# Kernel tuning notes

Measured on AMD Instinct MI355X. Metric: run time of the kernel, lower is better.

The kernel has to match this reference:

```python
import jax, jax.numpy as jnp
import numpy as np

C0, C1, ED, H, L, K = 128, 32, 64, 4, 2, 16
RADIUS = 16.0
EPS = 1e-6


def _ln(x, g, b):
    m = jnp.mean(x, -1, keepdims=True)
    v = jnp.var(x, -1, keepdims=True)
    return (x - m) * jax.lax.rsqrt(v + 1e-5) * g + b


def _gather_nodes(x, idx):
    # x [B,N,...], idx [B,N,K] -> [B,N,K,...]
    return jax.vmap(lambda xb, ib: xb[ib])(x, idx)


def _gather_pairs(e, idx):
    # e [B,N,N,ED], idx [B,N,K] -> [B,N,K,ED]  (batched_index_select on dim=2)
    return jax.vmap(lambda eb, ib: jnp.take_along_axis(eb, ib[..., None], axis=1))(e, idx)


def _fiber_norm(f0, f1, g0, b0, g1, b1):
    # deg-0: LayerNorm + gelu; deg-1: phase-preserving norm on channel magnitudes
    f0n = jax.nn.gelu(_ln(f0, g0, b0))
    n1 = jnp.linalg.norm(f1, axis=-1)                       # [B,N,C1]
    f1n = f1 / (n1 + EPS)[..., None] * jax.nn.gelu(_ln(n1, g1, b1))[..., None]
    return f0n, f1n


def _tfn_kv(f0j, f1j, y1, r, WA, WB):
    # Equivariant TFN edge kernel: paths 0->0(l=0), 1->0(l=1), 0->1(l=1),
    # 1->1(l=0), 1->1(l=1, cross), 1->1(l=2, traceless Y2) with radial gates r.
    r1, r2, r3, r4, r5, r6 = jnp.split(
        r, [C0, C0 + C1, 2 * C0 + C1, 2 * C0 + 2 * C1, 2 * C0 + 3 * C1], axis=-1)
    dot1 = jnp.einsum('bnkcm,bnkm->bnkc', f1j, y1)          # [B,N,K,C1]
    in0 = jnp.concatenate([r1 * f0j, r2 * dot1], -1)        # [B,N,K,C0+C1]
    k0 = jnp.einsum('oc,bnkc->bnko', WA, in0)               # [B,N,K,C0]
    p3 = (r3 * f0j)[..., None] * y1[..., None, :]           # [B,N,K,C0,3]
    p4 = r4[..., None] * f1j
    p5 = r5[..., None] * jnp.cross(f1j, y1[..., None, :])
    p6 = r6[..., None] * (y1[..., None, :] * dot1[..., None] - f1j / 3.0)
    in1 = jnp.concatenate([p3, p4, p5, p6], axis=-2)        # [B,N,K,C0+3*C1,3]
    k1 = jnp.einsum('oc,bnkcm->bnkom', WB, in1)             # [B,N,K,C1,3]
    return k0, k1


def reference(node_feats, pair_feats, coords, eln_g, eln_b, Wi0, Wi1,
              ln0_g, ln0_b, n1_g, n1_b, Wq0, Wq1, WrK, WrV, WkA, WkB, WvA, WvB,
              Wb, Wo0, Wo1, alpha_attn, lnf0_g, lnf0_b, nf1_g, nf1_b,
              Wf0a, Wf0b, Wf1a, Wf1b, alpha_ff, Wp0, Wp1):
    B, N = node_feats.shape[:2]
    Na, CA, Cc, Oo = [coords[..., i, :] for i in range(4)]          # each [B,N,3]
    f1_in = jnp.stack([Na, Cc, Oo], axis=-2) - CA[..., None, :]     # [B,N,3,3]
    # kNN graph on CA coords (exclude self), radius mask at 16A
    d2 = jnp.sum((CA[:, :, None] - CA[:, None, :]) ** 2, -1)        # [B,N,N]
    d2 = d2 + jnp.eye(N, dtype=d2.dtype) * 1e9
    nv, idx = jax.lax.top_k(-d2, K)                                 # idx [B,N,K]
    dist = jnp.sqrt(jnp.maximum(-nv, 0.0))
    mask = dist <= RADIUS
    rel_pos = _gather_nodes(CA, idx) - CA[:, :, None]               # [B,N,K,3]
    rel_b = jax.lax.stop_gradient(rel_pos)                          # basis on detached rel_pos
    y1 = rel_b / (jnp.linalg.norm(rel_b, axis=-1, keepdims=True) + EPS)
    edges = _ln(_gather_pairs(pair_feats, idx), eln_g, eln_b)       # [B,N,K,ED]
    # project in
    f0 = jnp.einsum('oc,bnc->bno', Wi0, node_feats)                 # [B,N,C0]
    f1 = jnp.einsum('oc,bncm->bnom', Wi1, f1_in)                    # [B,N,C1,3]
    dh0, dh1 = C0 // H, C1 // H
    scale = 1.0 / np.sqrt(dh0 + 3 * dh1)
    for l in range(L):
        # ---- attention block (prenorm -> TFN attention -> rezero residual)
        x0, x1 = _fiber_norm(f0, f1, ln0_g[l], ln0_b[l], n1_g[l], n1_b[l])
        q0 = jnp.einsum('oc,bnc->bno', Wq0[l], x0)
        q1 = jnp.einsum('oc,bncm->bnom', Wq1[l], x1)
        x0j = _gather_nodes(x0, idx)                                # [B,N,K,C0]
        x1j = _gather_nodes(x1, idx)                                # [B,N,K,C1,3]
        rk = jnp.einsum('re,bnke->bnkr', WrK[l], edges)
        rv = jnp.einsum('re,bnke->bnkr', WrV[l], edges)
        k0, k1 = _tfn_kv(x0j, x1j, y1, rk, WkA[l], WkB[l])
        v0, v1 = _tfn_kv(x0j, x1j, y1, rv, WvA[l], WvB[l])
        q0h = q0.reshape(B, N, H, dh0)
        q1h = q1.reshape(B, N, H, dh1, 3)
        k0h = k0.reshape(B, N, K, H, dh0)
        k1h = k1.reshape(B, N, K, H, dh1, 3)
        v0h = v0.reshape(B, N, K, H, dh0)
        v1h = v1.reshape(B, N, K, H, dh1, 3)
        logits = (jnp.einsum('bnhc,bnkhc->bnhk', q0h, k0h)
                  + jnp.einsum('bnhcm,bnkhcm->bnhk', q1h, k1h)) * scale
        logits = logits + jnp.einsum('he,bnke->bnhk', Wb[l], edges)
        logits = jnp.where(mask[:, :, None, :], logits, -1e9)
        attn = jax.nn.softmax(logits, axis=-1)
        o0 = jnp.einsum('bnhk,bnkhc->bnhc', attn, v0h).reshape(B, N, C0)
        o1 = jnp.einsum('bnhk,bnkhcm->bnhcm', attn, v1h).reshape(B, N, C1, 3)
        f0 = f0 + alpha_attn[l] * jnp.einsum('oc,bnc->bno', Wo0[l], o0)
        f1 = f1 + alpha_attn[l] * jnp.einsum('oc,bncm->bnom', Wo1[l], o1)
        # ---- fiber feedforward (prenorm -> FF -> rezero residual)
        x0, x1 = _fiber_norm(f0, f1, lnf0_g[l], lnf0_b[l], nf1_g[l], nf1_b[l])
        h0 = jnp.einsum('oh,bnh->bno', Wf0b[l],
                        jax.nn.gelu(jnp.einsum('hc,bnc->bnh', Wf0a[l], x0)))
        h1 = jnp.einsum('hc,bncm->bnhm', Wf1a[l], x1)
        nh = jnp.linalg.norm(h1, axis=-1)
        h1 = h1 * (jax.nn.gelu(nh) / (nh + EPS))[..., None]
        h1 = jnp.einsum('oh,bnhm->bnom', Wf1b[l], h1)
        f0 = f0 + alpha_ff[l] * h0
        f1 = f1 + alpha_ff[l] * h1
    # project out + _to_output
    node_out = jnp.einsum('oc,bnc->bno', Wp0, f0)                   # [B,N,128]
    coords_out = CA[:, :, None, :] + jnp.einsum('oc,bncm->bnom', Wp1, f1)  # [B,N,3,3]
    return node_out, coords_out


def setup_inputs() -> dict:
    key = jax.random.key(0)
    ks = iter(jax.random.split(key, 64))
    def rn(shape, scale=1.0):
        return (jax.random.normal(next(ks), shape) * scale).astype(jnp.float32)
    B, N = 1, 1024
    RC = 2 * C0 + 4 * C1
    ca = jnp.cumsum(rn((B, N, 3), 1.5), axis=1)          # protein-like chain
    coords = ca[:, :, None, :] + rn((B, N, 4, 3), 0.5)
    inp = dict(
        node_feats=rn((B, N, 128)),
        pair_feats=rn((B, N, N, ED)),
        coords=coords,
        eln_g=jnp.ones((ED,), jnp.float32), eln_b=jnp.zeros((ED,), jnp.float32),
        Wi0=rn((C0, 128), 128 ** -0.5), Wi1=rn((C1, 3), 3 ** -0.5),
        ln0_g=jnp.ones((L, C0), jnp.float32), ln0_b=jnp.zeros((L, C0), jnp.float32),
        n1_g=jnp.ones((L, C1), jnp.float32), n1_b=jnp.zeros((L, C1), jnp.float32),
        Wq0=rn((L, C0, C0), C0 ** -0.5), Wq1=rn((L, C1, C1), C1 ** -0.5),
        WrK=rn((L, RC, ED), ED ** -0.5), WrV=rn((L, RC, ED), ED ** -0.5),
        WkA=rn((L, C0, C0 + C1), (C0 + C1) ** -0.5),
        WkB=rn((L, C1, C0 + 3 * C1), (C0 + 3 * C1) ** -0.5),
        WvA=rn((L, C0, C0 + C1), (C0 + C1) ** -0.5),
        WvB=rn((L, C1, C0 + 3 * C1), (C0 + 3 * C1) ** -0.5),
        Wb=rn((L, H, ED), ED ** -0.5),
        Wo0=rn((L, C0, C0), C0 ** -0.5), Wo1=rn((L, C1, C1), C1 ** -0.5),
        alpha_attn=jnp.full((L,), 0.5, jnp.float32),
        lnf0_g=jnp.ones((L, C0), jnp.float32), lnf0_b=jnp.zeros((L, C0), jnp.float32),
        nf1_g=jnp.ones((L, C1), jnp.float32), nf1_b=jnp.zeros((L, C1), jnp.float32),
        Wf0a=rn((L, 4 * C0, C0), C0 ** -0.5), Wf0b=rn((L, C0, 4 * C0), (4 * C0) ** -0.5),
        Wf1a=rn((L, 4 * C1, C1), C1 ** -0.5), Wf1b=rn((L, C1, 4 * C1), (4 * C1) ** -0.5),
        alpha_ff=jnp.full((L,), 0.5, jnp.float32),
        Wp0=rn((128, C0), C0 ** -0.5), Wp1=rn((3, C1), C1 ** -0.5),
    )
    return inp
```

## Files before the change

kernel.cpp:

```cpp
#include <hip/hip_runtime.h>
#include <hip/hip_bf16.h>
#include <math.h>

static constexpr int NN  = 1024;
static constexpr int KK  = 16;
static constexpr int C0c = 128;
static constexpr int C1c = 32;
static constexpr int EDc = 64;
static constexpr int Lc  = 2;
static constexpr int ENUM = NN * KK;
static constexpr int PL   = NN * C1c;
static constexpr int X1HS = NN * 32;
#define SCALE_ATTN 0.13363062095621219f

typedef __attribute__((ext_vector_type(8))) short s8v;
typedef __attribute__((ext_vector_type(4))) float f4v;

__device__ __forceinline__ float wsum64(float v) {
    for (int o = 32; o > 0; o >>= 1) v += __shfl_xor(v, o);
    return v;
}
__device__ __forceinline__ float gsum16(float v) {
    for (int o = 8; o > 0; o >>= 1) v += __shfl_xor(v, o, 16);
    return v;
}
__device__ __forceinline__ float gmax16(float v) {
    for (int o = 8; o > 0; o >>= 1) v = fmaxf(v, __shfl_xor(v, o, 16));
    return v;
}
__device__ __forceinline__ float gelu_f(float x) {
    float x3 = x * x * x;
    return 0.5f * x * (1.0f + tanhf(0.7978845608028654f * (x + 0.044715f * x3)));
}
__device__ __forceinline__ unsigned short f2bf(float x) {
    union { float f; unsigned int u; } v; v.f = x;
    unsigned int r = v.u + 0x7fffu + ((v.u >> 16) & 1u);
    return (unsigned short)(r >> 16);
}
__device__ __forceinline__ float bf2f(unsigned short u) {
    union { float f; unsigned int i; } v; v.i = ((unsigned int)u) << 16;
    return v.f;
}
__device__ __forceinline__ s8v ld8(const unsigned short* p) { return *(const s8v*)p; }
__device__ __forceinline__ f4v mfma16(s8v a, s8v b, f4v c) {
    return __builtin_amdgcn_mfma_f32_16x16x32_bf16(a, b, c, 0, 0, 0);
}

struct CvJob { const float* s; unsigned short* d; int n; };
struct CvJobs { CvJob j[20]; int n; int total; };

__global__ __launch_bounds__(256) void setup_kernel(CvJobs cj, int cvb,
                                                    const float* __restrict__ coords,
                                                    int* __restrict__ idx,
                                                    float* __restrict__ maskf,
                                                    float* __restrict__ y1,
                                                    const float* __restrict__ Wi1,
                                                    float* __restrict__ f1p) {
    __shared__ float ca[NN * 3];
    const int tid = threadIdx.x;
    const int bx = blockIdx.x;
    if (bx < cvb) {
        int g = bx * 256 + tid;
        if (g >= cj.total) return;
        for (int i = 0; i < cj.n; ++i) {
            int n = cj.j[i].n;
            if (g < n) { cj.j[i].d[g] = f2bf(cj.j[i].s[g]); return; }
            g -= n;
        }
        return;
    }
    if (bx < cvb + 256) {
        for (int f = tid; f < NN * 3; f += 256) {
            int i = f / 3, m = f % 3;
            ca[f] = coords[(i * 4 + 1) * 3 + m];
        }
        __syncthreads();
        const int wid = tid >> 6, lane = tid & 63;
        const int n = (bx - cvb) * 4 + wid;
        const float cx = ca[n * 3 + 0], cy = ca[n * 3 + 1], cz = ca[n * 3 + 2];
        float d[16];
#pragma unroll
        for (int s = 0; s < 16; ++s) {
            int i = s * 64 + lane;
            float dx = cx - ca[i * 3 + 0], dy = cy - ca[i * 3 + 1], dz = cz - ca[i * 3 + 2];
            float d2 = dx * dx + dy * dy + dz * dz;
            d[s] = (i == n) ? 1e9f : d2;
        }
        for (int t = 0; t < KK; ++t) {
            float best = 1e30f; int bi = 0;
#pragma unroll
            for (int s = 0; s < 16; ++s) {
                int i = s * 64 + lane;
                float v = d[s];
                if (v < best || (v == best && i < bi)) { best = v; bi = i; }
            }
#pragma unroll
            for (int o = 32; o > 0; o >>= 1) {
                float ov = __shfl_xor(best, o);
                int   oi = __shfl_xor(bi, o);
                if (ov < best || (ov == best && oi < bi)) { best = ov; bi = oi; }
            }
            const int j = bi;
            if (lane == 0) {
                idx[n * KK + t] = j;
                float dist = sqrtf(best);
                maskf[n * KK + t] = (dist <= 16.0f) ? 1.0f : 0.0f;
                float rx = ca[j * 3 + 0] - cx, ry = ca[j * 3 + 1] - cy, rz = ca[j * 3 + 2] - cz;
                float nrm = sqrtf(rx * rx + ry * ry + rz * rz) + 1e-6f;
                y1[(n * KK + t) * 3 + 0] = rx / nrm;
                y1[(n * KK + t) * 3 + 1] = ry / nrm;
                y1[(n * KK + t) * 3 + 2] = rz / nrm;
            }
            const int js = j >> 6, jl = j & 63;
#pragma unroll
            for (int s = 0; s < 16; ++s)
                if (s == js && jl == lane) d[s] = 2e30f;
        }
        return;
    }
    int g = (bx - cvb - 256) * 256 + tid;
    if (g >= NN * 32) return;
    int n = g >> 5, c = g & 31;
    float w0 = Wi1[c * 3 + 0], w1 = Wi1[c * 3 + 1], w2 = Wi1[c * 3 + 2];
#pragma unroll
    for (int m = 0; m < 3; ++m) {
        float cav = coords[(n * 4 + 1) * 3 + m];
        float a0 = coords[(n * 4 + 0) * 3 + m] - cav;
        float a1 = coords[(n * 4 + 2) * 3 + m] - cav;
        float a2 = coords[(n * 4 + 3) * 3 + m] - cav;
        f1p[m * PL + n * 32 + c] = w0 * a0 + w1 * a1 + w2 * a2;
    }
}

__global__ __launch_bounds__(256) void edge_f0_kernel(const float* __restrict__ pair,
                                                      const int* __restrict__ idx,
                                                      const float* __restrict__ g,
                                                      const float* __restrict__ b,
                                                      const float* __restrict__ Wb,
                                                      unsigned short* __restrict__ edges_h,
                                                      float* __restrict__ biasb,
                                                      const unsigned short* __restrict__ nf_h,
                                                      const unsigned short* __restrict__ Wi0_h,
                                                      float* __restrict__ f0) {
    const int t = threadIdx.x, wid = t >> 6, lane = t & 63;
    if (blockIdx.x < ENUM / 4) {
        const int e = blockIdx.x * 4 + wid;
        const int n = e >> 4;
        const int j = idx[e];
        float v = pair[((size_t)n * NN + j) * EDc + lane];
        float m = wsum64(v) * (1.0f / 64.0f);
        float d = v - m;
        float var = wsum64(d * d) * (1.0f / 64.0f);
        float nv = d * rsqrtf(var + 1e-5f) * g[lane] + b[lane];
        edges_h[e * EDc + lane] = f2bf(nv);
#pragma unroll
        for (int l = 0; l < 2; ++l)
#pragma unroll
            for (int h = 0; h < 4; ++h) {
                float tt = wsum64(nv * Wb[(l * 4 + h) * 64 + lane]);
                if (lane == 0) biasb[(size_t)l * ENUM * 4 + e * 4 + h] = tt;
            }
        return;
    }
    int rel = blockIdx.x - ENUM / 4;
    const int mt = rel & 7, ntc = rel >> 3;
    const int m0 = mt * 128 + wid * 32, n0 = ntc * 32;
    const int c16 = lane & 15, g8 = (lane >> 4) * 8, g4 = (lane >> 4) * 4;
    f4v acc[2][2];
#pragma unroll
    for (int a = 0; a < 2; ++a)
#pragma unroll
        for (int bq = 0; bq < 2; ++bq) acc[a][bq] = f4v{0.f, 0.f, 0.f, 0.f};
    const unsigned short* Ap = nf_h + (size_t)(m0 + c16) * 128 + g8;
    const unsigned short* Bp = Wi0_h + (size_t)(n0 + c16) * 128 + g8;
#pragma unroll
    for (int kc = 0; kc < 128; kc += 32) {
        s8v a0 = ld8(Ap + kc);
        s8v a1 = ld8(Ap + 16 * 128 + kc);
        s8v b0 = ld8(Bp + kc);
        s8v b1 = ld8(Bp + 16 * 128 + kc);
        acc[0][0] = mfma16(a0, b0, acc[0][0]);
        acc[0][1] = mfma16(a0, b1, acc[0][1]);
        acc[1][0] = mfma16(a1, b0, acc[1][0]);
        acc[1][1] = mfma16(a1, b1, acc[1][1]);
    }
#pragma unroll
    for (int fm = 0; fm < 2; ++fm)
#pragma unroll
        for (int r = 0; r < 4; ++r) {
            const int m = m0 + fm * 16 + g4 + r;
#pragma unroll
            for (int fn = 0; fn < 2; ++fn)
                f0[(size_t)m * 128 + n0 + fn * 16 + c16] = acc[fm][fn][r];
        }
}

__global__ __launch_bounds__(256) void fnorm1_kernel(const float* __restrict__ f0,
                                                     const float* __restrict__ f1p,
                                                     const float* __restrict__ g0,
                                                     const float* __restrict__ b0,
                                                     const float* __restrict__ g1,
                                                     const float* __restrict__ b1,
                                                     unsigned short* __restrict__ x0h,
                                                     unsigned short* __restrict__ x1h) {
    const int wid = threadIdx.x >> 6, lane = threadIdx.x & 63;
    const int n = blockIdx.x * 4 + wid;
    float va = f0[n * 128 + lane], vb = f0[n * 128 + lane + 64];
    float m = wsum64(va + vb) * (1.0f / 128.0f);
    float da = va - m, db = vb - m;
    float var = wsum64(da * da + db * db) * (1.0f / 128.0f);
    float rs = rsqrtf(var + 1e-5f);
    x0h[n * 128 + lane]      = f2bf(gelu_f(da * rs * g0[lane] + b0[lane]));
    x0h[n * 128 + lane + 64] = f2bf(gelu_f(db * rs * g0[lane + 64] + b0[lane + 64]));
    int c = lane & 31;
    float h0 = f1p[0 * PL + n * 32 + c];
    float h1 = f1p[1 * PL + n * 32 + c];
    float h2 = f1p[2 * PL + n * 32 + c];
    float n1 = sqrtf(h0 * h0 + h1 * h1 + h2 * h2);
    float ms = wsum64(n1) * (1.0f / 64.0f);
    float dd = n1 - ms;
    float vv = wsum64(dd * dd) * (1.0f / 64.0f);
    float sc = gelu_f(dd * rsqrtf(vv + 1e-5f) * g1[c] + b1[c]) / (n1 + 1e-6f);
    if (lane < 32) {
        x1h[0 * X1HS + n * 32 + c] = f2bf(h0 * sc);
        x1h[1 * X1HS + n * 32 + c] = f2bf(h1 * sc);
        x1h[2 * X1HS + n * 32 + c] = f2bf(h2 * sc);
    }
}

static constexpr int EKV_LDS = (64 * 168 + 64 * 136 + 3 * 64 * 104) * 2;

__global__ __launch_bounds__(256) void edge_kv_kernel(
    const unsigned short* __restrict__ edges_h,
    const unsigned short* __restrict__ WrK, const unsigned short* __restrict__ WrV,
    const unsigned short* __restrict__ WkA, const unsigned short* __restrict__ WvA,
    const unsigned short* __restrict__ WkB, const unsigned short* __restrict__ WvB,
    const unsigned short* __restrict__ x0h, const unsigned short* __restrict__ x1h,
    const int* __restrict__ idx, const float* __restrict__ y1,
    unsigned short* __restrict__ k0h, unsigned short* __restrict__ v0h,
    unsigned short* __restrict__ uKh, unsigned short* __restrict__ uVh,
    unsigned short* __restrict__ k1ph, unsigned short* __restrict__ v1ph,
    const unsigned short* __restrict__ Wq0l, const unsigned short* __restrict__ Wq1l,
    float* __restrict__ q0, float* __restrict__ q1p) {
    extern __shared__ unsigned short lsm[];
    const int t = threadIdx.x, w = t >> 6, l = t & 63;
    const int c16 = l & 15, g8 = (l >> 4) * 8, g4 = (l >> 4) * 4;
    const int bid = blockIdx.x;
    if (bid < 512) {
        unsigned short* in0L = lsm;
        unsigned short* inUL = lsm + 64 * 168;
        unsigned short* inWL = lsm + 64 * 168 + 64 * 136;
        const int s = bid >> 8, et = bid & 255, e0 = et * 64;
        const unsigned short* Wr = s ? WrV : WrK;
        const unsigned short* WA = s ? WvA : WkA;
        const unsigned short* WB = s ? WvB : WkB;
        unsigned short* K0o = s ? v0h : k0h;
        unsigned short* Uo  = s ? uVh : uKh;
        unsigned short* K1o = s ? v1ph : k1ph;
#pragma unroll 1
        for (int ti = w; ti < 24; ti += 4) {
            const int esub = ti & 1, rt = ti >> 1;
            const int e0w = e0 + esub * 32, r0 = rt * 32;
            f4v acc[2][2];
#pragma unroll
            for (int a = 0; a < 2; ++a)
#pragma unroll
                for (int bq = 0; bq < 2; ++bq) acc[a][bq] = f4v{0.f, 0.f, 0.f, 0.f};
#pragma unroll
            for (int kc = 0; kc < 64; kc += 32) {
                s8v a0 = ld8(edges_h + (size_t)(e0w + c16) * 64 + kc + g8);
                s8v a1 = ld8(edges_h + (size_t)(e0w + 16 + c16) * 64 + kc + g8);
                s8v b0 = ld8(Wr + (size_t)(r0 + c16) * 64 + kc + g8);
                s8v b1 = ld8(Wr + (size_t)(r0 + 16 + c16) * 64 + kc + g8);
                acc[0][0] = mfma16(a0, b0, acc[0][0]);
                acc[0][1] = mfma16(a0, b1, acc[0][1]);
                acc[1][0] = mfma16(a1, b0, acc[1][0]);
                acc[1][1] = mfma16(a1, b1, acc[1][1]);
            }
#pragma unroll
            for (int fm = 0; fm < 2; ++fm)
#pragma unroll
                for (int r = 0; r < 4; ++r) {
                    const int el = esub * 32 + fm * 16 + g4 + r;
                    const int e = e0 + el;
                    const int j = idx[e];
                    float ya = y1[e * 3 + 0], yb = y1[e * 3 + 1], yc = y1[e * 3 + 2];
#pragma unroll
                    for (int fn = 0; fn < 2; ++fn) {
                        const float av = acc[fm][fn][r];
                        const int col = r0 + fn * 16 + c16;
                        if (r0 < 128) {
                            in0L[el * 168 + col] = f2bf(av * bf2f(x0h[j * 128 + col]));
                        } else if (r0 < 160) {
                            int c = col - 128;
                            float d1 = bf2f(x1h[0 * X1HS + j * 32 + c]) * ya
                                     + bf2f(x1h[1 * X1HS + j * 32 + c]) * yb
                                     + bf2f(x1h[2 * X1HS + j * 32 + c]) * yc;
                            in0L[el * 168 + col] = f2bf(av * d1);
                        } else if (r0 < 288) {
                            int c = col - 160;
                            inUL[el * 136 + c] = f2bf(av * bf2f(x0h[j * 128 + c]));
                        } else {
                            int c = (r0 < 320) ? (col - 288) : (r0 < 352) ? (col - 320) : (col - 352);
                            float fx = bf2f(x1h[0 * X1HS + j * 32 + c]);
                            float fy = bf2f(x1h[1 * X1HS + j * 32 + c]);
                            float fz = bf2f(x1h[2 * X1HS + j * 32 + c]);
                            float w0, w1, w2; int off;
                            if (r0 < 320) {
                                off = 0; w0 = av * fx; w1 = av * fy; w2 = av * fz;
                            } else if (r0 < 352) {
                                off = 32;
                                w0 = av * (fy * yc - fz * yb);
                                w1 = av * (fz * ya - fx * yc);
                                w2 = av * (fx * yb - fy * ya);
                            } else {
                                off = 64;
                                float d1 = fx * ya + fy * yb + fz * yc;
                                w0 = av * (ya * d1 - fx * (1.0f / 3.0f));
                                w1 = av * (yb * d1 - fy * (1.0f / 3.0f));
                                w2 = av * (yc * d1 - fz * (1.0f / 3.0f));
                            }
                            inWL[0 * 64 * 104 + el * 104 + off + c] = f2bf(w0);
                            inWL[1 * 64 * 104 + el * 104 + off + c] = f2bf(w1);
                            inWL[2 * 64 * 104 + el * 104 + off + c] = f2bf(w2);
                        }
                    }
                }
        }
        __syncthreads();
#pragma unroll 1
        for (int ti = w; ti < 16; ti += 4) {
            const unsigned short* Ab; const unsigned short* Bb;
            unsigned short* Cb;
            int apit, K, ldb, ldcq, esub;
            if (ti < 8) {
                esub = ti & 1; int nt = ti >> 1;
                Ab = in0L; apit = 168; K = 160;
                Bb = WA + (size_t)(nt * 32) * 160; ldb = 160;
                Cb = K0o + (size_t)(e0 + esub * 32) * 128 + nt * 32; ldcq = 128;
            } else if (ti < 10) {
                esub = ti - 8;
                Ab = inUL; apit = 136; K = 128; Bb = WB; ldb = 224;
                Cb = Uo + (size_t)(e0 + esub * 32) * 32; ldcq = 32;
            } else {
                int id = ti - 10; int m = id >> 1; esub = id & 1;
                Ab = inWL + m * 64 * 104; apit = 104; K = 96;
                Bb = WB + 128; ldb = 224;
                Cb = K1o + ((size_t)m * ENUM + e0 + esub * 32) * 32; ldcq = 32;
            }
            const int m0l = esub * 32;
            f4v acc[2][2];
#pragma unroll
            for (int a = 0; a < 2; ++a)
#pragma unroll
                for (int bq = 0; bq < 2; ++bq) acc[a][bq] = f4v{0.f, 0.f, 0.f, 0.f};
            for (int kc = 0; kc < K; kc += 32) {
                s8v a0 = *(const s8v*)&Ab[(m0l + c16) * apit + kc + g8];
                s8v a1 = *(const s8v*)&Ab[(m0l + 16 + c16) * apit + kc + g8];
                s8v b0 = ld8(Bb + (size_t)c16 * ldb + kc + g8);
                s8v b1 = ld8(Bb + (size_t)(16 + c16) * ldb + kc + g8);
                acc[0][0] = mfma16(a0, b0, acc[0][0]);
                acc[0][1] = mfma16(a0, b1, acc[0][1]);
                acc[1][0] = mfma16(a1, b0, acc[1][0]);
                acc[1][1] = mfma16(a1, b1, acc[1][1]);
            }
#pragma unroll
            for (int fm = 0; fm < 2; ++fm)
#pragma unroll
                for (int r = 0; r < 4; ++r) {
                    const int lr = fm * 16 + g4 + r;
#pragma unroll
                    for (int fn = 0; fn < 2; ++fn)
                        Cb[(size_t)lr * ldcq + fn * 16 + c16] = f2bf(acc[fm][fn][r]);
                }
        }
        return;
    }
    const int rel = bid - 512;
    const unsigned short* A; const unsigned short* B;
    float* C; int K, lda2, ldb2, ldc2, m0, n0;
    if (rel < 32) {
        int mt = rel & 7, nt = rel >> 3;
        A = x0h; B = Wq0l; C = q0;
        K = 128; lda2 = 128; ldb2 = 128; ldc2 = 128;
        m0 = mt * 128 + w * 32; n0 = nt * 32;
    } else {
        int k = rel - 32; int pl = k >> 3; int mt = k & 7;
        A = x1h + (size_t)pl * X1HS; B = Wq1l; C = q1p + (size_t)pl * PL;
        K = 32; lda2 = 32; ldb2 = 32; ldc2 = 32;
        m0 = mt * 128 + w * 32; n0 = 0;
    }
    f4v acc[2][2];
#pragma unroll
    for (int a = 0; a < 2; ++a)
#pragma unroll
        for (int bq = 0; bq < 2; ++bq) acc[a][bq] = f4v{0.f, 0.f, 0.f, 0.f};
    const unsigned short* Ap = A + (size_t)(m0 + c16) * lda2 + g8;
    const unsigned short* Bp = B + (size_t)(n0 + c16) * ldb2 + g8;
    for (int kc = 0; kc < K; kc += 32) {
        s8v a0 = ld8(Ap + kc);
        s8v a1 = ld8(Ap + 16 * lda2 + kc);
        s8v b0 = ld8(Bp + kc);
        s8v b1 = ld8(Bp + 16 * ldb2 + kc);
        acc[0][0] = mfma16(a0, b0, acc[0][0]);
        acc[0][1] = mfma16(a0, b1, acc[0][1]);
        acc[1][0] = mfma16(a1, b0, acc[1][0]);
        acc[1][1] = mfma16(a1, b1, acc[1][1]);
    }
#pragma unroll
    for (int fm = 0; fm < 2; ++fm)
#pragma unroll
        for (int r = 0; r < 4; ++r) {
            const int m = m0 + fm * 16 + g4 + r;
#pragma unroll
            for (int fn = 0; fn < 2; ++fn)
                C[(size_t)m * ldc2 + n0 + fn * 16 + c16] = acc[fm][fn][r];
        }
}

__global__ __launch_bounds__(256) void attn_core(const float* __restrict__ q0,
                                                 const float* __restrict__ q1p,
                                                 const unsigned short* __restrict__ k0h,
                                                 const unsigned short* __restrict__ k1ph,
                                                 const unsigned short* __restrict__ v0h,
                                                 const unsigned short* __restrict__ v1ph,
                                                 const unsigned short* __restrict__ uKh,
                                                 const unsigned short* __restrict__ uVh,
                                                 const float* __restrict__ biasb,
                                                 const float* __restrict__ maskf,
                                                 const float* __restrict__ y1,
                                                 unsigned short* __restrict__ o0h,
                                                 unsigned short* __restrict__ o1h) {
    __shared__ float q0s[4][128];
    __shared__ float q1s[4][96];
    __shared__ float attns[4][64];
    const int wid = threadIdx.x >> 6, lane = threadIdx.x & 63;
    const int n = blockIdx.x * 4 + wid;
    q0s[wid][lane]      = q0[n * 128 + lane];
    q0s[wid][lane + 64] = q0[n * 128 + lane + 64];
    if (lane < 32) {
#pragma unroll
        for (int m = 0; m < 3; ++m) q1s[wid][m * 32 + lane] = q1p[m * PL + n * 32 + lane];
    }
    __syncthreads();
    const int h = lane >> 4, k = lane & 15;
    const int e = n * KK + k;
    float acc = 0.f;
    const unsigned short* kr = k0h + (size_t)e * 128 + h * 32;
#pragma unroll
    for (int c8 = 0; c8 < 4; ++c8) {
        s8v kv = ld8(kr + c8 * 8);
#pragma unroll
        for (int j = 0; j < 8; ++j)
            acc += q0s[wid][h * 32 + c8 * 8 + j] * bf2f((unsigned short)kv[j]);
    }
    float yv[3] = {y1[e * 3 + 0], y1[e * 3 + 1], y1[e * 3 + 2]};
#pragma unroll
    for (int m = 0; m < 3; ++m) {
        const unsigned short* k1r = k1ph + ((size_t)m * ENUM + e) * 32 + h * 8;
        const unsigned short* ur  = uKh + (size_t)e * 32 + h * 8;
#pragma unroll
        for (int c = 0; c < 8; ++c)
            acc += q1s[wid][m * 32 + h * 8 + c] * (bf2f(k1r[c]) + bf2f(ur[c]) * yv[m]);
    }
    acc = acc * SCALE_ATTN + biasb[e * 4 + h];
    if (maskf[e] == 0.0f) acc = -1e9f;
    float mx = gmax16(acc);
    float ex = expf(acc - mx);
    float sm = gsum16(ex);
    attns[wid][lane] = ex / sm;
    __syncthreads();
#pragma unroll
    for (int t = 0; t < 2; ++t) {
        int oc = lane + 64 * t;
        int h2 = oc >> 5;
        float a = 0.f;
        for (int kk = 0; kk < KK; ++kk)
            a += attns[wid][h2 * 16 + kk] * bf2f(v0h[(size_t)(n * KK + kk) * 128 + oc]);
        o0h[(size_t)n * 128 + oc] = f2bf(a);
    }
    for (int val = lane; val < 96; val += 64) {
        int cc = val & 31, m = val >> 5;
        int h2 = cc >> 3;
        float a = 0.f;
        for (int kk = 0; kk < KK; ++kk) {
            int e2 = n * KK + kk;
            a += attns[wid][h2 * 16 + kk] *
                 (bf2f(v1ph[((size_t)m * ENUM + e2) * 32 + cc]) +
                  bf2f(uVh[(size_t)e2 * 32 + cc]) * y1[e2 * 3 + m]);
        }
        o1h[((size_t)m * NN + n) * 32 + cc] = f2bf(a);
    }
}

template <int MODE>
__global__ __launch_bounds__(256) void fused_post(
    const unsigned short* __restrict__ o0h, const unsigned short* __restrict__ o1h,
    float* __restrict__ f0, float* __restrict__ f1p,
    const unsigned short* __restrict__ Wo0h, const unsigned short* __restrict__ Wo1h,
    const unsigned short* __restrict__ Wf0ah, const unsigned short* __restrict__ Wf0bh,
    const unsigned short* __restrict__ Wf1ah, const unsigned short* __restrict__ Wf1bh,
    const float* __restrict__ alA, const float* __restrict__ alF,
    const float* __restrict__ lnf0_g, const float* __restrict__ lnf0_b,
    const float* __restrict__ nf1_g, const float* __restrict__ nf1_b,
    const float* __restrict__ ln0n_g, const float* __restrict__ ln0n_b,
    const float* __restrict__ n1n_g, const float* __restrict__ n1n_b,
    unsigned short* __restrict__ x0h, unsigned short* __restrict__ x1h,
    const unsigned short* __restrict__ Wp0h, const float* __restrict__ Wp1,
    const float* __restrict__ coords, float* __restrict__ out) {
    __shared__ float f0s[16][132];
    __shared__ float f1s[3][16][36];
    __shared__ unsigned short x0s[16][136];
    __shared__ float x1s[3][16][36];
    __shared__ unsigned short hs[16][520];
    __shared__ unsigned short h1b[3][16][136];
    const int t = threadIdx.x, w = t >> 6, l = t & 63;
    const int c16 = l & 15, g8 = (l >> 4) * 8, g4 = (l >> 4) * 4;
    const int n0 = blockIdx.x * 16;
    const float aA = alA[0], aF = alF[0];

    {
        f4v acc[2] = {f4v{0.f,0.f,0.f,0.f}, f4v{0.f,0.f,0.f,0.f}};
        const unsigned short* Ap = o0h + (size_t)(n0 + c16) * 128 + g8;
#pragma unroll
        for (int kc = 0; kc < 128; kc += 32) {
            s8v a = ld8(Ap + kc);
#pragma unroll
            for (int tt = 0; tt < 2; ++tt) {
                s8v b = ld8(Wo0h + (size_t)((w * 2 + tt) * 16 + c16) * 128 + g8 + kc);
                acc[tt] = mfma16(a, b, acc[tt]);
            }
        }
#pragma unroll
        for (int tt = 0; tt < 2; ++tt) {
            int colg = (w * 2 + tt) * 16 + c16;
#pragma unroll
            for (int r = 0; r < 4; ++r) {
                int row = g4 + r;
                f0s[row][colg] = f0[(size_t)(n0 + row) * 128 + colg] + aA * acc[tt][r];
            }
        }
    }
#pragma unroll
    for (int it = 0; it < 6; ++it) {
        int g = t + it * 256;
        int c = g & 31, node = (g >> 5) & 15, m = g >> 9;
        float a = 0.f;
        const unsigned short* wrow = Wo1h + c * 32;
        const unsigned short* orow = o1h + ((size_t)m * NN + n0 + node) * 32;
#pragma unroll
        for (int cc = 0; cc < 32; ++cc) a += bf2f(wrow[cc]) * bf2f(orow[cc]);
        f1s[m][node][c] = f1p[(size_t)m * PL + (n0 + node) * 32 + c] + aA * a;
    }
    __syncthreads();
    for (int i = 0; i < 4; ++i) {
        int row = w * 4 + i;
        float v0 = f0s[row][l], v1 = f0s[row][l + 64];
        float mn = wsum64(v0 + v1) * (1.0f / 128.0f);
        float d0 = v0 - mn, d1 = v1 - mn;
        float var = wsum64(d0 * d0 + d1 * d1) * (1.0f / 128.0f);
        float rs = rsqrtf(var + 1e-5f);
        x0s[row][l]      = f2bf(gelu_f(d0 * rs * lnf0_g[l] + lnf0_b[l]));
        x0s[row][l + 64] = f2bf(gelu_f(d1 * rs * lnf0_g[l + 64] + lnf0_b[l + 64]));
    }
    {
        int node = t >> 4, sub = t & 15;
        float p[2][3], n1v[2];
#pragma unroll
        for (int q = 0; q < 2; ++q) {
            int c = sub + q * 16;
            p[q][0] = f1s[0][node][c]; p[q][1] = f1s[1][node][c]; p[q][2] = f1s[2][node][c];
            n1v[q] = sqrtf(p[q][0]*p[q][0] + p[q][1]*p[q][1] + p[q][2]*p[q][2]);
        }
        float s = gsum16(n1v[0] + n1v[1]);
        float mn = s * (1.0f / 32.0f);
        float d0 = n1v[0] - mn, d1 = n1v[1] - mn;
        float vv = gsum16(d0 * d0 + d1 * d1);
        float rs = rsqrtf(vv * (1.0f / 32.0f) + 1e-5f);
#pragma unroll
        for (int q = 0; q < 2; ++q) {
            int c = sub + q * 16;
            float sc = gelu_f((n1v[q] - mn) * rs * nf1_g[c] + nf1_b[c]) / (n1v[q] + 1e-6f);
            x1s[0][node][c] = p[q][0] * sc;
            x1s[1][node][c] = p[q][1] * sc;
            x1s[2][node][c] = p[q][2] * sc;
        }
    }
    __syncthreads();
    {
        f4v acc[8];
#pragma unroll
        for (int i = 0; i < 8; ++i) acc[i] = f4v{0.f,0.f,0.f,0.f};
#pragma unroll
        for (int kc = 0; kc < 128; kc += 32) {
            s8v a = *(const s8v*)&x0s[c16][kc + g8];
#pragma unroll
            for (int tt = 0; tt < 8; ++tt) {
                s8v b = ld8(Wf0ah + (size_t)((w * 8 + tt) * 16 + c16) * 128 + g8 + kc);
                acc[tt] = mfma16(a, b, acc[tt]);
            }
        }
#pragma unroll
        for (int tt = 0; tt < 8; ++tt) {
            int colg = (w * 8 + tt) * 16 + c16;
#pragma unroll
            for (int r = 0; r < 4; ++r) hs[g4 + r][colg] = f2bf(gelu_f(acc[tt][r]));
        }
    }
#pragma unroll
    for (int it = 0; it < 8; ++it) {
        int g = t + it * 256;
        int r = g & 127, node = g >> 7;
        float a0 = 0.f, a1 = 0.f, a2 = 0.f;
        const unsigned short* wrow = Wf1ah + r * 32;
#pragma unroll
        for (int c = 0; c < 32; ++c) {
            float wv = bf2f(wrow[c]);
            a0 += wv * x1s[0][node][c];
            a1 += wv * x1s[1][node][c];
            a2 += wv * x1s[2][node][c];
        }
        float nh = sqrtf(a0 * a0 + a1 * a1 + a2 * a2);
        float sc = gelu_f(nh) / (nh + 1e-6f);
        h1b[0][node][r] = f2bf(a0 * sc);
        h1b[1][node][r] = f2bf(a1 * sc);
        h1b[2][node][r] = f2bf(a2 * sc);
    }
    __syncthreads();
    {
        f4v acc[2] = {f4v{0.f,0.f,0.f,0.f}, f4v{0.f,0.f,0.f,0.f}};
#pragma unroll 4
        for (int kc = 0; kc < 512; kc += 32) {
            s8v a = *(const s8v*)&hs[c16][kc + g8];
#pragma unroll
            for (int tt = 0; tt < 2; ++tt) {
                s8v b = ld8(Wf0bh + (size_t)((w * 2 + tt) * 16 + c16) * 512 + g8 + kc);
                acc[tt] = mfma16(a, b, acc[tt]);
            }
        }
#pragma unroll
        for (int tt = 0; tt < 2; ++tt) {
            int colg = (w * 2 + tt) * 16 + c16;
#pragma unroll
            for (int r = 0; r < 4; ++r) {
                int row = g4 + r;
                float v = f0s[row][colg] + aF * acc[tt][r];
                f0s[row][colg] = v;
                f0[(size_t)(n0 + row) * 128 + colg] = v;
            }
        }
    }
#pragma unroll
    for (int it = 0; it < 6; ++it) {
        int g = t + it * 256;
        int c = g & 31, node = (g >> 5) & 15, m = g >> 9;
        float a = 0.f;
        const unsigned short* wrow = Wf1bh + c * 128;
#pragma unroll 8
        for (int r = 0; r < 128; ++r) a += bf2f(wrow[r]) * bf2f(h1b[m][node][r]);
        float v = f1s[m][node][c] + aF * a;
        f1s[m][node][c] = v;
        f1p[(size_t)m * PL + (n0 + node) * 32 + c] = v;
    }
    __syncthreads();
    if (MODE == 0) {
        for (int i = 0; i < 4; ++i) {
            int row = w * 4 + i;
            float v0 = f0s[row][l], v1 = f0s[row][l + 64];
            float mn = wsum64(v0 + v1) * (1.0f / 128.0f);
            float d0 = v0 - mn, d1 = v1 - mn;
            float var = wsum64(d0 * d0 + d1 * d1) * (1.0f / 128.0f);
            float rs = rsqrtf(var + 1e-5f);
            x0h[(size_t)(n0 + row) * 128 + l]      = f2bf(gelu_f(d0 * rs * ln0n_g[l] + ln0n_b[l]));
            x0h[(size_t)(n0 + row) * 128 + l + 64] = f2bf(gelu_f(d1 * rs * ln0n_g[l + 64] + ln0n_b[l + 64]));
        }
        {
            int node = t >> 4, sub = t & 15;
            float p[2][3], n1v[2];
#pragma unroll
            for (int q = 0; q < 2; ++q) {
                int c = sub + q * 16;
                p[q][0] = f1s[0][node][c]; p[q][1] = f1s[1][node][c]; p[q][2] = f1s[2][node][c];
                n1v[q] = sqrtf(p[q][0]*p[q][0] + p[q][1]*p[q][1] + p[q][2]*p[q][2]);
            }
            float s = gsum16(n1v[0] + n1v[1]);
            float mn = s * (1.0f / 32.0f);
            float d0 = n1v[0] - mn, d1 = n1v[1] - mn;
            float vv = gsum16(d0 * d0 + d1 * d1);
            float rs = rsqrtf(vv * (1.0f / 32.0f) + 1e-5f);
#pragma unroll
            for (int q = 0; q < 2; ++q) {
                int c = sub + q * 16;
                float sc = gelu_f((n1v[q] - mn) * rs * n1n_g[c] + n1n_b[c]) / (n1v[q] + 1e-6f);
                x1h[(size_t)0 * X1HS + (n0 + node) * 32 + c] = f2bf(p[q][0] * sc);
                x1h[(size_t)1 * X1HS + (n0 + node) * 32 + c] = f2bf(p[q][1] * sc);
                x1h[(size_t)2 * X1HS + (n0 + node) * 32 + c] = f2bf(p[q][2] * sc);
            }
        }
    } else {
#pragma unroll
        for (int it = 0; it < 8; ++it) {
            int g = t + it * 256;
            int row = g >> 7, col = g & 127;
            x0s[row][col] = f2bf(f0s[row][col]);
        }
        __syncthreads();
        f4v acc[2] = {f4v{0.f,0.f,0.f,0.f}, f4v{0.f,0.f,0.f,0.f}};
#pragma unroll
        for (int kc = 0; kc < 128; kc += 32) {
            s8v a = *(const s8v*)&x0s[c16][kc + g8];
#pragma unroll
            for (int tt = 0; tt < 2; ++tt) {
                s8v b = ld8(Wp0h + (size_t)((w * 2 + tt) * 16 + c16) * 128 + g8 + kc);
                acc[tt] = mfma16(a, b, acc[tt]);
            }
        }
#pragma unroll
        for (int tt = 0; tt < 2; ++tt) {
            int colg = (w * 2 + tt) * 16 + c16;
#pragma unroll
            for (int r = 0; r < 4; ++r)
                out[(size_t)(n0 + g4 + r) * 128 + colg] = acc[tt][r];
        }
        if (t < 144) {
            int node = t / 9, rr = t % 9, o = rr / 3, m = rr % 3;
            float a = coords[((size_t)(n0 + node) * 4 + 1) * 3 + m];
            for (int c = 0; c < 32; ++c) a += Wp1[o * 32 + c] * f1s[m][node][c];
            out[NN * 128 + ((size_t)(n0 + node) * 3 + o) * 3 + m] = a;
        }
    }
}

extern "C" void kernel_launch(void* const* d_in, const int* in_sizes, int n_in,
                              void* d_out, int out_size, void* d_ws, size_t ws_size,
                              hipStream_t stream) {
    (void)in_sizes; (void)n_in; (void)out_size; (void)ws_size;
    const float* node_feats = (const float*)d_in[0];
    const float* pair       = (const float*)d_in[1];
    const float* coords     = (const float*)d_in[2];
    const float* eln_g      = (const float*)d_in[3];
    const float* eln_b      = (const float*)d_in[4];
    const float* Wi0        = (const float*)d_in[5];
    const float* Wi1        = (const float*)d_in[6];
    const float* ln0_g      = (const float*)d_in[7];
    const float* ln0_b      = (const float*)d_in[8];
    const float* n1_g       = (const float*)d_in[9];
    const float* n1_b       = (const float*)d_in[10];
    const float* Wq0        = (const float*)d_in[11];
    const float* Wq1        = (const float*)d_in[12];
    const float* WrK        = (const float*)d_in[13];
    const float* WrV        = (const float*)d_in[14];
    const float* WkA        = (const float*)d_in[15];
    const float* WkB        = (const float*)d_in[16];
    const float* WvA        = (const float*)d_in[17];
    const float* WvB        = (const float*)d_in[18];
    const float* Wb         = (const float*)d_in[19];
    const float* Wo0        = (const float*)d_in[20];
    const float* Wo1        = (const float*)d_in[21];
    const float* alpha_attn = (const float*)d_in[22];
    const float* lnf0_g     = (const float*)d_in[23];
    const float* lnf0_b     = (const float*)d_in[24];
    const float* nf1_g      = (const float*)d_in[25];
    const float* nf1_b      = (const float*)d_in[26];
    const float* Wf0a       = (const float*)d_in[27];
    const float* Wf0b       = (const float*)d_in[28];
    const float* Wf1a       = (const float*)d_in[29];
    const float* Wf1b       = (const float*)d_in[30];
    const float* alpha_ff   = (const float*)d_in[31];
    const float* Wp0        = (const float*)d_in[32];
    const float* Wp1        = (const float*)d_in[33];
    float* out = (float*)d_out;

    float* ws = (float*)d_ws;
    size_t off = 0;
    int*   idx   = (int*)(ws + off); off += NN * KK;
    float* maskf = ws + off;         off += NN * KK;
    float* y1    = ws + off;         off += NN * KK * 3;
    float* f0    = ws + off;         off += NN * C0c;
    float* f1p   = ws + off;         off += 3 * PL;
    float* q0    = ws + off;         off += NN * C0c;
    float* q1p   = ws + off;         off += 3 * PL;
    float* biasb = ws + off;         off += (size_t)2 * ENUM * 4;
    off = (off + 3) & ~(size_t)3;
    unsigned short* up = (unsigned short*)(ws + off);
    size_t uo = 0;
    unsigned short* edges_h = up + uo; uo += (size_t)ENUM * 64;
    unsigned short* x0h     = up + uo; uo += (size_t)NN * 128;
    unsigned short* x1h     = up + uo; uo += (size_t)3 * X1HS;
    unsigned short* nf_h    = up + uo; uo += (size_t)NN * 128;
    unsigned short* k0h     = up + uo; uo += (size_t)ENUM * 128;
    unsigned short* v0h     = up + uo; uo += (size_t)ENUM * 128;
    unsigned short* uKh     = up + uo; uo += (size_t)ENUM * 32;
    unsigned short* uVh     = up + uo; uo += (size_t)ENUM * 32;
    unsigned short* k1ph    = up + uo; uo += (size_t)3 * ENUM * 32;
    unsigned short* v1ph    = up + uo; uo += (size_t)3 * ENUM * 32;
    unsigned short* o0h     = up + uo; uo += (size_t)NN * 128;
    unsigned short* o1h     = up + uo; uo += (size_t)3 * NN * 32;
    unsigned short* WrK_h   = up + uo; uo += 2 * 24576;
    unsigned short* WrV_h   = up + uo; uo += 2 * 24576;
    unsigned short* WkA_h   = up + uo; uo += 2 * 20480;
    unsigned short* WvA_h   = up + uo; uo += 2 * 20480;
    unsigned short* WkB_h   = up + uo; uo += 2 * 7168;
    unsigned short* WvB_h   = up + uo; uo += 2 * 7168;
    unsigned short* Wq0_h   = up + uo; uo += 2 * 16384;
    unsigned short* Wq1_h   = up + uo; uo += 2 * 1024;
    unsigned short* Wo0_h   = up + uo; uo += 2 * 16384;
    unsigned short* Wo1_h   = up + uo; uo += 2 * 1024;
    unsigned short* Wf0a_h  = up + uo; uo += 2 * 65536;
    unsigned short* Wf0b_h  = up + uo; uo += 2 * 65536;
    unsigned short* Wf1a_h  = up + uo; uo += 2 * 4096;
    unsigned short* Wf1b_h  = up + uo; uo += 2 * 4096;
    unsigned short* Wp0_h   = up + uo; uo += 16384;
    unsigned short* Wi0_h   = up + uo; uo += 16384;

    CvJobs cj; cj.n = 17;
    cj.j[0]  = {WrK,  WrK_h,  2 * 24576};
    cj.j[1]  = {WrV,  WrV_h,  2 * 24576};
    cj.j[2]  = {WkA,  WkA_h,  2 * 20480};
    cj.j[3]  = {WvA,  WvA_h,  2 * 20480};
    cj.j[4]  = {WkB,  WkB_h,  2 * 7168};
    cj.j[5]  = {WvB,  WvB_h,  2 * 7168};
    cj.j[6]  = {Wq0,  Wq0_h,  2 * 16384};
    cj.j[7]  = {Wq1,  Wq1_h,  2 * 1024};
    cj.j[8]  = {Wo0,  Wo0_h,  2 * 16384};
    cj.j[9]  = {Wo1,  Wo1_h,  2 * 1024};
    cj.j[10] = {Wf0a, Wf0a_h, 2 * 65536};
    cj.j[11] = {Wf0b, Wf0b_h, 2 * 65536};
    cj.j[12] = {Wf1a, Wf1a_h, 2 * 4096};
    cj.j[13] = {Wf1b, Wf1b_h, 2 * 4096};
    cj.j[14] = {Wp0,  Wp0_h,  16384};
    cj.j[15] = {Wi0,  Wi0_h,  16384};
    cj.j[16] = {node_feats, nf_h, NN * 128};
    cj.total = 2*24576*2 + 2*20480*2 + 2*7168*2 + 2*16384 + 2*1024 + 2*16384
             + 2*1024 + 2*65536*2 + 2*4096*2 + 16384 + 16384 + NN*128;
    const int cvb = (cj.total + 255) / 256;

    setup_kernel<<<cvb + 256 + 128, 256, 0, stream>>>(cj, cvb, coords, idx, maskf, y1, Wi1, f1p);
    edge_f0_kernel<<<ENUM / 4 + 32, 256, 0, stream>>>(pair, idx, eln_g, eln_b, Wb,
                                                      edges_h, biasb, nf_h, Wi0_h, f0);
    fnorm1_kernel<<<NN / 4, 256, 0, stream>>>(f0, f1p, ln0_g, ln0_b, n1_g, n1_b, x0h, x1h);

    for (int l = 0; l < Lc; ++l) {
        edge_kv_kernel<<<568, 256, EKV_LDS, stream>>>(
            edges_h,
            WrK_h + (size_t)l * 24576, WrV_h + (size_t)l * 24576,
            WkA_h + (size_t)l * 20480, WvA_h + (size_t)l * 20480,
            WkB_h + (size_t)l * 7168,  WvB_h + (size_t)l * 7168,
            x0h, x1h, idx, y1,
            k0h, v0h, uKh, uVh, k1ph, v1ph,
            Wq0_h + (size_t)l * 16384, Wq1_h + (size_t)l * 1024, q0, q1p);
        attn_core<<<NN / 4, 256, 0, stream>>>(q0, q1p, k0h, k1ph, v0h, v1ph, uKh, uVh,
            biasb + (size_t)l * ENUM * 4, maskf, y1, o0h, o1h);
        if (l == 0) {
            fused_post<0><<<NN / 16, 256, 0, stream>>>(
                o0h, o1h, f0, f1p,
                Wo0_h, Wo1_h, Wf0a_h, Wf0b_h, Wf1a_h, Wf1b_h,
                alpha_attn + 0, alpha_ff + 0,
                lnf0_g, lnf0_b, nf1_g, nf1_b,
                ln0_g + 128, ln0_b + 128, n1_g + 32, n1_b + 32,
                x0h, x1h, nullptr, nullptr, nullptr, nullptr);
        } else {
            fused_post<1><<<NN / 16, 256, 0, stream>>>(
                o0h, o1h, f0, f1p,
                Wo0_h + 16384, Wo1_h + 1024, Wf0a_h + 65536, Wf0b_h + 65536,
                Wf1a_h + 4096, Wf1b_h + 4096,
                alpha_attn + 1, alpha_ff + 1,
                lnf0_g + 128, lnf0_b + 128, nf1_g + 32, nf1_b + 32,
                nullptr, nullptr, nullptr, nullptr,
                nullptr, nullptr, Wp0_h, Wp1, coords, out);
        }
    }
}
```

Measured before the change: 268.2 us.

## Vectorize attention value aggregation and widen fused_post blocks to 512 threads

In attn_core, the weighted sum over neighbours is reorganized. Each lane now loads 8 bf16 values with vector loads over a quarter of the neighbours, the partial sums are reduced across lane groups with shuffles, and results are written as packed 8-wide stores. This replaces the earlier scalar strided loads. In fused_post, block size doubles to 512 threads with 8 waves, and each wave owns fewer MFMA output tiles and rows, giving more parallelism per block since only 64 blocks launch. The cost is more shuffles and idle lanes in the o1 path, plus higher per-block resource use.

```diff
diff --git a/kernel.cpp b/kernel.cpp
--- a/kernel.cpp
+++ b/kernel.cpp
@@ -443,58 +443,94 @@
         for (int m = 0; m < 3; ++m) q1s[wid][m * 32 + lane] = q1p[m * PL + n * 32 + lane];
     }
     __syncthreads();
-    const int h = lane >> 4, k = lane & 15;
-    const int e = n * KK + k;
-    float acc = 0.f;
-    const unsigned short* kr = k0h + (size_t)e * 128 + h * 32;
-#pragma unroll
-    for (int c8 = 0; c8 < 4; ++c8) {
-        s8v kv = ld8(kr + c8 * 8);
-#pragma unroll
-        for (int j = 0; j < 8; ++j)
-            acc += q0s[wid][h * 32 + c8 * 8 + j] * bf2f((unsigned short)kv[j]);
-    }
-    float yv[3] = {y1[e * 3 + 0], y1[e * 3 + 1], y1[e * 3 + 2]};
-#pragma unroll
-    for (int m = 0; m < 3; ++m) {
-        const unsigned short* k1r = k1ph + ((size_t)m * ENUM + e) * 32 + h * 8;
-        const unsigned short* ur  = uKh + (size_t)e * 32 + h * 8;
-#pragma unroll
-        for (int c = 0; c < 8; ++c)
-            acc += q1s[wid][m * 32 + h * 8 + c] * (bf2f(k1r[c]) + bf2f(ur[c]) * yv[m]);
-    }
-    acc = acc * SCALE_ATTN + biasb[e * 4 + h];
-    if (maskf[e] == 0.0f) acc = -1e9f;
-    float mx = gmax16(acc);
-    float ex = expf(acc - mx);
-    float sm = gsum16(ex);
-    attns[wid][lane] = ex / sm;
+    {
+        const int h = lane >> 4, k = lane & 15;
+        const int e = n * KK + k;
+        float acc = 0.f;
+        const unsigned short* kr = k0h + (size_t)e * 128 + h * 32;
+#pragma unroll
+        for (int c8 = 0; c8 < 4; ++c8) {
+            s8v kv = ld8(kr + c8 * 8);
+#pragma unroll
+            for (int j = 0; j < 8; ++j)
+                acc += q0s[wid][h * 32 + c8 * 8 + j] * bf2f((unsigned short)kv[j]);
+        }
+        s8v uv = ld8(uKh + (size_t)e * 32 + h * 8);
+#pragma unroll
+        for (int m = 0; m < 3; ++m) {
+            float yv = y1[e * 3 + m];
+            s8v k1v = ld8(k1ph + ((size_t)m * ENUM + e) * 32 + h * 8);
+#pragma unroll
+            for (int c = 0; c < 8; ++c)
+                acc += q1s[wid][m * 32 + h * 8 + c] *
+                       (bf2f((unsigned short)k1v[c]) + bf2f((unsigned short)uv[c]) * yv);
+        }
+        acc = acc * SCALE_ATTN + biasb[e * 4 + h];
+        if (maskf[e] == 0.0f) acc = -1e9f;
+        float mx = gmax16(acc);
+        float ex = expf(acc - mx);
+        float sm = gsum16(ex);
+        attns[wid][lane] = ex / sm;
+    }
     __syncthreads();
-#pragma unroll
-    for (int t = 0; t < 2; ++t) {
-        int oc = lane + 64 * t;
-        int h2 = oc >> 5;
-        float a = 0.f;
-        for (int kk = 0; kk < KK; ++kk)
-            a += attns[wid][h2 * 16 + kk] * bf2f(v0h[(size_t)(n * KK + kk) * 128 + oc]);
-        o0h[(size_t)n * 128 + oc] = f2bf(a);
-    }
-    for (int val = lane; val < 96; val += 64) {
-        int cc = val & 31, m = val >> 5;
-        int h2 = cc >> 3;
-        float a = 0.f;
-        for (int kk = 0; kk < KK; ++kk) {
-            int e2 = n * KK + kk;
-            a += attns[wid][h2 * 16 + kk] *
-                 (bf2f(v1ph[((size_t)m * ENUM + e2) * 32 + cc]) +
-                  bf2f(uVh[(size_t)e2 * 32 + cc]) * y1[e2 * 3 + m]);
-        }
-        o1h[((size_t)m * NN + n) * 32 + cc] = f2bf(a);
+    const int g = lane & 15, kq = lane >> 4;
+    {
+        float o[8] = {};
+        const float* aw = &attns[wid][(g >> 2) * 16];
+#pragma unroll
+        for (int kk2 = 0; kk2 < 4; ++kk2) {
+            int kk = kq * 4 + kk2;
+            float a = aw[kk];
+            s8v v = ld8(v0h + (size_t)(n * KK + kk) * 128 + g * 8);
+#pragma unroll
+            for (int j = 0; j < 8; ++j) o[j] += a * bf2f((unsigned short)v[j]);
+        }
+#pragma unroll
+        for (int j = 0; j < 8; ++j) {
+            o[j] += __shfl_xor(o[j], 16);
+            o[j] += __shfl_xor(o[j], 32);
+        }
+        if (kq == 0) {
+            s8v r;
+#pragma unroll
+            for (int j = 0; j < 8; ++j) r[j] = (short)f2bf(o[j]);
+            *(s8v*)&o0h[(size_t)n * 128 + g * 8] = r;
+        }
+    }
+    {
+        float o[8] = {};
+        const int plane = g >> 2, cg = g & 3;
+        if (g < 12) {
+            const float* aw = &attns[wid][cg * 16];
+#pragma unroll
+            for (int kk2 = 0; kk2 < 4; ++kk2) {
+                int kk = kq * 4 + kk2;
+                int e2 = n * KK + kk;
+                float a = aw[kk];
+                float yv = y1[e2 * 3 + plane];
+                s8v v = ld8(v1ph + ((size_t)plane * ENUM + e2) * 32 + cg * 8);
+                s8v u = ld8(uVh + (size_t)e2 * 32 + cg * 8);
+#pragma unroll
+                for (int j = 0; j < 8; ++j)
+                    o[j] += a * (bf2f((unsigned short)v[j]) + bf2f((unsigned short)u[j]) * yv);
+            }
+        }
+#pragma unroll
+        for (int j = 0; j < 8; ++j) {
+            o[j] += __shfl_xor(o[j], 16);
+            o[j] += __shfl_xor(o[j], 32);
+        }
+        if (kq == 0 && g < 12) {
+            s8v r;
+#pragma unroll
+            for (int j = 0; j < 8; ++j) r[j] = (short)f2bf(o[j]);
+            *(s8v*)&o1h[((size_t)plane * NN + n) * 32 + cg * 8] = r;
+        }
     }
 }
 
 template <int MODE>
-__global__ __launch_bounds__(256) void fused_post(
+__global__ __launch_bounds__(512) void fused_post(
     const unsigned short* __restrict__ o0h, const unsigned short* __restrict__ o1h,
     float* __restrict__ f0, float* __restrict__ f1p,
     const unsigned short* __restrict__ Wo0h, const unsigned short* __restrict__ Wo1h,
@@ -520,30 +556,24 @@
     const float aA = alA[0], aF = alF[0];
 
     {
-        f4v acc[2] = {f4v{0.f,0.f,0.f,0.f}, f4v{0.f,0.f,0.f,0.f}};
+        f4v acc = f4v{0.f, 0.f, 0.f, 0.f};
         const unsigned short* Ap = o0h + (size_t)(n0 + c16) * 128 + g8;
 #pragma unroll
         for (int kc = 0; kc < 128; kc += 32) {
             s8v a = ld8(Ap + kc);
-#pragma unroll
-            for (int tt = 0; tt < 2; ++tt) {
-                s8v b = ld8(Wo0h + (size_t)((w * 2 + tt) * 16 + c16) * 128 + g8 + kc);
-                acc[tt] = mfma16(a, b, acc[tt]);
-            }
-        }
-#pragma unroll
-        for (int tt = 0; tt < 2; ++tt) {
-            int colg = (w * 2 + tt) * 16 + c16;
-#pragma unroll
-            for (int r = 0; r < 4; ++r) {
-                int row = g4 + r;
-                f0s[row][colg] = f0[(size_t)(n0 + row) * 128 + colg] + aA * acc[tt][r];
-            }
-        }
-    }
-#pragma unroll
-    for (int it = 0; it < 6; ++it) {
-        int g = t + it * 256;
+            s8v b = ld8(Wo0h + (size_t)(w * 16 + c16) * 128 + g8 + kc);
+            acc = mfma16(a, b, acc);
+        }
+        int colg = w * 16 + c16;
+#pragma unroll
+        for (int r = 0; r < 4; ++r) {
+            int row = g4 + r;
+            f0s[row][colg] = f0[(size_t)(n0 + row) * 128 + colg] + aA * acc[r];
+        }
+    }
+#pragma unroll
+    for (int it = 0; it < 3; ++it) {
+        int g = t + it * 512;
         int c = g & 31, node = (g >> 5) & 15, m = g >> 9;
         float a = 0.f;
         const unsigned short* wrow = Wo1h + c * 32;
@@ -553,8 +583,8 @@
         f1s[m][node][c] = f1p[(size_t)m * PL + (n0 + node) * 32 + c] + aA * a;
     }
     __syncthreads();
-    for (int i = 0; i < 4; ++i) {
-        int row = w * 4 + i;
+    for (int i = 0; i < 2; ++i) {
+        int row = w * 2 + i;
         float v0 = f0s[row][l], v1 = f0s[row][l + 64];
         float mn = wsum64(v0 + v1) * (1.0f / 128.0f);
         float d0 = v0 - mn, d1 = v1 - mn;
@@ -563,7 +593,7 @@
         x0s[row][l]      = f2bf(gelu_f(d0 * rs * lnf0_g[l] + lnf0_b[l]));
         x0s[row][l + 64] = f2bf(gelu_f(d1 * rs * lnf0_g[l + 64] + lnf0_b[l + 64]));
     }
-    {
+    if (t < 256) {
         int node = t >> 4, sub = t & 15;
         float p[2][3], n1v[2];
 #pragma unroll
@@ -588,28 +618,28 @@
     }
     __syncthreads();
     {
-        f4v acc[8];
-#pragma unroll
-        for (int i = 0; i < 8; ++i) acc[i] = f4v{0.f,0.f,0.f,0.f};
+        f4v acc[4];
+#pragma unroll
+        for (int i = 0; i < 4; ++i) acc[i] = f4v{0.f,0.f,0.f,0.f};
 #pragma unroll
         for (int kc = 0; kc < 128; kc += 32) {
             s8v a = *(const s8v*)&x0s[c16][kc + g8];
 #pragma unroll
-            for (int tt = 0; tt < 8; ++tt) {
-                s8v b = ld8(Wf0ah + (size_t)((w * 8 + tt) * 16 + c16) * 128 + g8 + kc);
+            for (int tt = 0; tt < 4; ++tt) {
+                s8v b = ld8(Wf0ah + (size_t)((w * 4 + tt) * 16 + c16) * 128 + g8 + kc);
                 acc[tt] = mfma16(a, b, acc[tt]);
             }
         }
 #pragma unroll
-        for (int tt = 0; tt < 8; ++tt) {
-            int colg = (w * 8 + tt) * 16 + c16;
+        for (int tt = 0; tt < 4; ++tt) {
+            int colg = (w * 4 + tt) * 16 + c16;
 #pragma unroll
             for (int r = 0; r < 4; ++r) hs[g4 + r][colg] = f2bf(gelu_f(acc[tt][r]));
         }
     }
 #pragma unroll
-    for (int it = 0; it < 8; ++it) {
-        int g = t + it * 256;
+    for (int it = 0; it < 4; ++it) {
+        int g = t + it * 512;
         int r = g & 127, node = g >> 7;
         float a0 = 0.f, a1 = 0.f, a2 = 0.f;
         const unsigned short* wrow = Wf1ah + r * 32;
@@ -628,31 +658,25 @@
     }
     __syncthreads();
     {
-        f4v acc[2] = {f4v{0.f,0.f,0.f,0.f}, f4v{0.f,0.f,0.f,0.f}};
+        f4v acc = f4v{0.f, 0.f, 0.f, 0.f};
 #pragma unroll 4
         for (int kc = 0; kc < 512; kc += 32) {
             s8v a = *(const s8v*)&hs[c16][kc + g8];
-#pragma unroll
-            for (int tt = 0; tt < 2; ++tt) {
-                s8v b = ld8(Wf0bh + (size_t)((w * 2 + tt) * 16 + c16) * 512 + g8 + kc);
-                acc[tt] = mfma16(a, b, acc[tt]);
-            }
-        }
-#pragma unroll
-        for (int tt = 0; tt < 2; ++tt) {
-            int colg = (w * 2 + tt) * 16 + c16;
-#pragma unroll
-            for (int r = 0; r < 4; ++r) {
-                int row = g4 + r;
-                float v = f0s[row][colg] + aF * acc[tt][r];
-                f0s[row][colg] = v;
-                f0[(size_t)(n0 + row) * 128 + colg] = v;
-            }
-        }
-    }
-#pragma unroll
-    for (int it = 0; it < 6; ++it) {
-        int g = t + it * 256;
+            s8v b = ld8(Wf0bh + (size_t)(w * 16 + c16) * 512 + g8 + kc);
+            acc = mfma16(a, b, acc);
+        }
+        int colg = w * 16 + c16;
+#pragma unroll
+        for (int r = 0; r < 4; ++r) {
+            int row = g4 + r;
+            float v = f0s[row][colg] + aF * acc[r];
+            f0s[row][colg] = v;
+            f0[(size_t)(n0 + row) * 128 + colg] = v;
+        }
+    }
+#pragma unroll
+    for (int it = 0; it < 3; ++it) {
+        int g = t + it * 512;
         int c = g & 31, node = (g >> 5) & 15, m = g >> 9;
         float a = 0.f;
         const unsigned short* wrow = Wf1bh + c * 128;
@@ -664,8 +688,8 @@
     }
     __syncthreads();
     if (MODE == 0) {
-        for (int i = 0; i < 4; ++i) {
-            int row = w * 4 + i;
+        for (int i = 0; i < 2; ++i) {
+            int row = w * 2 + i;
             float v0 = f0s[row][l], v1 = f0s[row][l + 64];
             float mn = wsum64(v0 + v1) * (1.0f / 128.0f);
             float d0 = v0 - mn, d1 = v1 - mn;
@@ -674,7 +698,7 @@
             x0h[(size_t)(n0 + row) * 128 + l]      = f2bf(gelu_f(d0 * rs * ln0n_g[l] + ln0n_b[l]));
             x0h[(size_t)(n0 + row) * 128 + l + 64] = f2bf(gelu_f(d1 * rs * ln0n_g[l + 64] + ln0n_b[l + 64]));
         }
-        {
+        if (t < 256) {
             int node = t >> 4, sub = t & 15;
             float p[2][3], n1v[2];
 #pragma unroll
@@ -699,29 +723,23 @@
         }
     } else {
 #pragma unroll
-        for (int it = 0; it < 8; ++it) {
-            int g = t + it * 256;
+        for (int it = 0; it < 4; ++it) {
+            int g = t + it * 512;
             int row = g >> 7, col = g & 127;
             x0s[row][col] = f2bf(f0s[row][col]);
         }
         __syncthreads();
-        f4v acc[2] = {f4v{0.f,0.f,0.f,0.f}, f4v{0.f,0.f,0.f,0.f}};
+        f4v acc = f4v{0.f, 0.f, 0.f, 0.f};
 #pragma unroll
         for (int kc = 0; kc < 128; kc += 32) {
             s8v a = *(const s8v*)&x0s[c16][kc + g8];
-#pragma unroll
-            for (int tt = 0; tt < 2; ++tt) {
-                s8v b = ld8(Wp0h + (size_t)((w * 2 + tt) * 16 + c16) * 128 + g8 + kc);
-                acc[tt] = mfma16(a, b, acc[tt]);
-            }
-        }
-#pragma unroll
-        for (int tt = 0; tt < 2; ++tt) {
-            int colg = (w * 2 + tt) * 16 + c16;
-#pragma unroll
-            for (int r = 0; r < 4; ++r)
-                out[(size_t)(n0 + g4 + r) * 128 + colg] = acc[tt][r];
-        }
+            s8v b = ld8(Wp0h + (size_t)(w * 16 + c16) * 128 + g8 + kc);
+            acc = mfma16(a, b, acc);
+        }
+        int colg = w * 16 + c16;
+#pragma unroll
+        for (int r = 0; r < 4; ++r)
+            out[(size_t)(n0 + g4 + r) * 128 + colg] = acc[r];
         if (t < 144) {
             int node = t / 9, rr = t % 9, o = rr / 3, m = rr % 3;
             float a = coords[((size_t)(n0 + node) * 4 + 1) * 3 + m];
@@ -852,7 +870,7 @@
         attn_core<<<NN / 4, 256, 0, stream>>>(q0, q1p, k0h, k1ph, v0h, v1ph, uKh, uVh,
             biasb + (size_t)l * ENUM * 4, maskf, y1, o0h, o1h);
         if (l == 0) {
-            fused_post<0><<<NN / 16, 256, 0, stream>>>(
+            fused_post<0><<<NN / 16, 512, 0, stream>>>(
                 o0h, o1h, f0, f1p,
                 Wo0_h, Wo1_h, Wf0a_h, Wf0b_h, Wf1a_h, Wf1b_h,
                 alpha_attn + 0, alpha_ff + 0,
@@ -860,7 +878,7 @@
                 ln0_g + 128, ln0_b + 128, n1_g + 32, n1_b + 32,
                 x0h, x1h, nullptr, nullptr, nullptr, nullptr);
         } else {
-            fused_post<1><<<NN / 16, 256, 0, stream>>>(
+            fused_post<1><<<NN / 16, 512, 0, stream>>>(
                 o0h, o1h, f0, f1p,
                 Wo0_h + 16384, Wo1_h + 1024, Wf0a_h + 65536, Wf0b_h + 65536,
                 Wf1a_h + 4096, Wf1b_h + 4096,
```

After: 242.6 us. 9.5% less time.
